# Kernel tuning notes

Hardware: AMD Instinct MI355X
Metric: run time of the kernel (lower is better)

## Reference

```python
import jax, jax.numpy as jnp
import numpy as np

B, N, F = 8, 512, 128
H, U = 4, 32
LEAKY_ALPHA = 0.2

def setup_inputs() -> dict:
    key = jax.random.key(0)
    k1, k2, k3, k4 = jax.random.split(key, 4)
    inputs = jax.random.normal(k1, (B, N, F), dtype=jnp.float32)
    # glorot-ish scaled params
    W_src = jax.random.normal(k2, (H, F, U), dtype=jnp.float32) * (2.0 / (F + U)) ** 0.5
    W_dst = jax.random.normal(k3, (H, F, U), dtype=jnp.float32) * (2.0 / (F + U)) ** 0.5
    a = jax.random.normal(k4, (H, U, 1), dtype=jnp.float32) * (2.0 / (U + 1)) ** 0.5
    return {"inputs": inputs, "W_src": W_src, "W_dst": W_dst, "a": a}

def reference(inputs, W_src, W_dst, a):
    # GATv2, eval mode (no dropout). Loop over the small fixed head count to
    # keep peak memory at one (B,N,N,U) pairwise tensor at a time, matching
    # the original per-head loop.
    outs = []
    for h in range(W_src.shape[0]):
        h_src = inputs @ W_src[h]          # (B, N, U)
        h_dst = inputs @ W_dst[h]          # (B, N, U)
        # pairwise[b,i,j,:] = h_src[b,i] + h_dst[b,j]
        pair = jax.nn.leaky_relu(h_src[:, :, None, :] + h_dst[:, None, :, :],
                                 negative_slope=LEAKY_ALPHA)  # (B,N,N,U)
        scores = jnp.einsum('biju,u->bij', pair, a[h, :, 0])   # (B,N,N)
        attn = jax.nn.softmax(scores, axis=-1)
        outs.append(attn @ h_src)          # (B,N,U) -- weighted sum of h_src
    return jnp.concatenate(outs, axis=-1)  # concat_heads=True -> (B,N,H*U)
```

## Files before the change

kernel.cpp:

```cpp
#include <hip/hip_runtime.h>
#include <hip/hip_bf16.h>

#define B_ 8
#define N_ 512
#define F_ 128
#define H_ 4
#define U_ 32
#define LEAKY_ALPHA 0.2f
#define PS 520

typedef __attribute__((ext_vector_type(8))) short short8;
typedef __attribute__((ext_vector_type(4))) short short4v;
typedef __attribute__((ext_vector_type(4))) float f32x4;

static __device__ __forceinline__ short f2bf_s(float x) {
    __hip_bfloat16 hv = __float2bfloat16(x);
    return *reinterpret_cast<short*>(&hv);
}
static __device__ __forceinline__ float bf2f_s(short v) {
    return __uint_as_float(((unsigned)(unsigned short)v) << 16);
}

__global__ __launch_bounds__(512) void proj_kernel(
    const float* __restrict__ x, const float* __restrict__ Wsrc,
    const float* __restrict__ Wdst, const float* __restrict__ a,
    float* __restrict__ hsrc, float* __restrict__ hdstNT,
    float* __restrict__ Drow, float* __restrict__ ascaled,
    short* __restrict__ hsrcT)
{
    __shared__ float4 xlds[16 * 32];
    const int t  = threadIdx.x;
    const int r0 = blockIdx.x * 16;

    xlds[t] = ((const float4*)x)[(size_t)r0 * 32 + t];
    __syncthreads();

    const int u  = t & 31;
    const int h  = (t >> 5) & 3;
    const int rq = t >> 7;
    const float* Ws = Wsrc + h * (F_ * U_) + u;
    const float* Wd = Wdst + h * (F_ * U_) + u;

    float as[4], ad[4];
#pragma unroll
    for (int r = 0; r < 4; ++r) { as[r] = 0.f; ad[r] = 0.f; }

#pragma unroll 2
    for (int fc = 0; fc < 32; ++fc) {
        const float s0 = Ws[(4 * fc + 0) * U_];
        const float s1 = Ws[(4 * fc + 1) * U_];
        const float s2 = Ws[(4 * fc + 2) * U_];
        const float s3 = Ws[(4 * fc + 3) * U_];
        const float d0 = Wd[(4 * fc + 0) * U_];
        const float d1 = Wd[(4 * fc + 1) * U_];
        const float d2 = Wd[(4 * fc + 2) * U_];
        const float d3 = Wd[(4 * fc + 3) * U_];
#pragma unroll
        for (int r = 0; r < 4; ++r) {
            const float4 xv = xlds[(rq * 4 + r) * 32 + fc];
            float vs = as[r], vd = ad[r];
            vs = fmaf(xv.x, s0, vs);  vd = fmaf(xv.x, d0, vd);
            vs = fmaf(xv.y, s1, vs);  vd = fmaf(xv.y, d1, vd);
            vs = fmaf(xv.z, s2, vs);  vd = fmaf(xv.z, d2, vd);
            vs = fmaf(xv.w, s3, vs);  vd = fmaf(xv.w, d3, vd);
            as[r] = vs; ad[r] = vd;
        }
    }

    const float av = a[h * U_ + u];
    if (t < 128 && blockIdx.x == 0)
        ascaled[h * U_ + u] = (1.f - LEAKY_ALPHA) * av;

    const int b  = r0 >> 9;
    const int n0 = (r0 & (N_ - 1)) + rq * 4;
    const int bh = b * H_ + h;

    short4v pk;
#pragma unroll
    for (int r = 0; r < 4; ++r) {
        hsrc[((size_t)(bh * N_ + n0 + r) << 5) + u] = as[r];
        pk[r] = f2bf_s(as[r]);
    }
    *(short4v*)&hsrcT[((size_t)(bh * U_) + u) * N_ + n0] = pk;

    float4 nv;
    nv.x = -ad[0]; nv.y = -ad[1]; nv.z = -ad[2]; nv.w = -ad[3];
    *(float4*)&hdstNT[((size_t)(bh * U_) + u) * N_ + n0] = nv;

#pragma unroll
    for (int r = 0; r < 4; ++r) {
        float v = ad[r] * av;
        v += __shfl_xor(v, 1);
        v += __shfl_xor(v, 2);
        v += __shfl_xor(v, 4);
        v += __shfl_xor(v, 8);
        v += __shfl_xor(v, 16);
        if (u == 0) Drow[bh * N_ + n0 + r] = v;
    }
}

__global__ __launch_bounds__(512, 4) void attn_kernel(
    const float* __restrict__ hsrc, const float* __restrict__ hdstNT,
    const float* __restrict__ Drow, const float* __restrict__ ascaled,
    const short* __restrict__ hsrcT, float* __restrict__ out)
{
    __shared__ __align__(16) short pbf[16 * PS];
    __shared__ f32x4 scr[8][64];
    __shared__ float lfin[16];

    const int t    = threadIdx.x;
    const int L    = t & 63;
    const int w    = __builtin_amdgcn_readfirstlane(t >> 6);
    const int tile = blockIdx.x & 31;
    const int bh   = blockIdx.x >> 5;
    const int h    = bh & 3;
    const int b    = bh >> 2;
    const size_t bhN = (size_t)bh * N_;
    const int ig0  = tile * 16;
    const int j    = t;

    const float* sB = hsrc + ((bhN + ig0) << 5);

    {
        const float warm = sB[t];
        asm volatile("" :: "v"(warm));
    }

    const float* dT = hdstNT + ((size_t)bh * U_) * N_ + j;
#define DL(k) float d##k = dT[(k) * N_];
    DL(0) DL(1) DL(2) DL(3) DL(4) DL(5) DL(6) DL(7)
    DL(8) DL(9) DL(10) DL(11) DL(12) DL(13) DL(14) DL(15)
    DL(16) DL(17) DL(18) DL(19) DL(20) DL(21) DL(22) DL(23)
    DL(24) DL(25) DL(26) DL(27) DL(28) DL(29) DL(30) DL(31)
#undef DL
#define PIN4(a0,a1,a2,a3) asm volatile("" : "+v"(a0), "+v"(a1), "+v"(a2), "+v"(a3));
    PIN4(d0,d1,d2,d3)     PIN4(d4,d5,d6,d7)
    PIN4(d8,d9,d10,d11)   PIN4(d12,d13,d14,d15)
    PIN4(d16,d17,d18,d19) PIN4(d20,d21,d22,d23)
    PIN4(d24,d25,d26,d27) PIN4(d28,d29,d30,d31)
#undef PIN4

    const float Dj = Drow[bhN + j];
    const float* aS = ascaled + h * U_;

#define TERM(k, dk, accv) accv = fmaf(aS[k], fmaxf(sR[k], dk), accv);
#pragma unroll 2
    for (int i = 0; i < 16; ++i) {
        const float* sR = sB + (i << 5);
        float acA = 0.f, acB = 0.f;
        TERM(0,  d0,  acA) TERM(1,  d1,  acB) TERM(2,  d2,  acA) TERM(3,  d3,  acB)
        TERM(4,  d4,  acA) TERM(5,  d5,  acB) TERM(6,  d6,  acA) TERM(7,  d7,  acB)
        TERM(8,  d8,  acA) TERM(9,  d9,  acB) TERM(10, d10, acA) TERM(11, d11, acB)
        TERM(12, d12, acA) TERM(13, d13, acB) TERM(14, d14, acA) TERM(15, d15, acB)
        TERM(16, d16, acA) TERM(17, d17, acB) TERM(18, d18, acA) TERM(19, d19, acB)
        TERM(20, d20, acA) TERM(21, d21, acB) TERM(22, d22, acA) TERM(23, d23, acB)
        TERM(24, d24, acA) TERM(25, d25, acB) TERM(26, d26, acA) TERM(27, d27, acB)
        TERM(28, d28, acA) TERM(29, d29, acB) TERM(30, d30, acA) TERM(31, d31, acB)
        const float e = __expf(Dj + acA + acB);
        pbf[i * PS + j] = f2bf_s(e);
    }
#undef TERM
    __syncthreads();

    {
        const int ri = t >> 5;
        const int rg = t & 31;
        const short8* pr = (const short8*)(pbf + ri * PS + rg * 16);
        const short8 pa = pr[0];
        const short8 pb = pr[1];
        float sum = 0.f;
#pragma unroll
        for (int k = 0; k < 8; ++k) sum += bf2f_s(pa[k]) + bf2f_s(pb[k]);
        sum += __shfl_xor(sum, 1);
        sum += __shfl_xor(sum, 2);
        sum += __shfl_xor(sum, 4);
        sum += __shfl_xor(sum, 8);
        sum += __shfl_xor(sum, 16);
        if (rg == 0) lfin[ri] = __builtin_amdgcn_rcpf(sum);
    }

    const int m  = L & 15;
    const int kq = L >> 4;
    const int nt = w & 1;
    const int ks = w >> 1;
    const short* Ap = pbf + m * PS + ks * 128 + kq * 8;
    const short* Bp = hsrcT + ((size_t)bh * U_ + nt * 16 + m) * N_ + ks * 128 + kq * 8;

    f32x4 acc = {0.f, 0.f, 0.f, 0.f};
#pragma unroll
    for (int st = 0; st < 4; ++st) {
        const short8 af = *(const short8*)(Ap + st * 32);
        const short8 bf = *(const short8*)(Bp + st * 32);
        acc = __builtin_amdgcn_mfma_f32_16x16x32_bf16(af, bf, acc, 0, 0, 0);
    }
    scr[w][L] = acc;
    __syncthreads();

    if (w < 2) {
        f32x4 s0 = scr[w][L];
        const f32x4 s1 = scr[w + 2][L];
        const f32x4 s2 = scr[w + 4][L];
        const f32x4 s3 = scr[w + 6][L];
        s0 += s1; s0 += s2; s0 += s3;
#pragma unroll
        for (int r = 0; r < 4; ++r) {
            const int il = kq * 4 + r;
            out[((size_t)(b * N_ + ig0 + il)) * (H_ * U_) + h * U_ + w * 16 + m]
                = s0[r] * lfin[il];
        }
    }
}

extern "C" void kernel_launch(void* const* d_in, const int* in_sizes, int n_in,
                              void* d_out, int out_size, void* d_ws, size_t ws_size,
                              hipStream_t stream) {
    const float* x    = (const float*)d_in[0];
    const float* Wsrc = (const float*)d_in[1];
    const float* Wdst = (const float*)d_in[2];
    const float* a    = (const float*)d_in[3];

    float* ws      = (float*)d_ws;
    float* hsrc    = ws;
    float* hdstNT  = hsrc + (size_t)B_ * H_ * N_ * U_;
    float* Drow    = hdstNT + (size_t)B_ * H_ * U_ * N_;
    float* ascaled = Drow + (size_t)B_ * H_ * N_;
    short* hsrcT   = (short*)(ascaled + H_ * U_);

    proj_kernel<<<(B_ * N_) / 16, 512, 0, stream>>>(x, Wsrc, Wdst, a,
                                                    hsrc, hdstNT, Drow, ascaled,
                                                    hsrcT);
    attn_kernel<<<B_ * H_ * (N_ / 16), 512, 0, stream>>>(hsrc, hdstNT, Drow,
                                                         ascaled, hsrcT,
                                                         (float*)d_out);
}
```

Baseline: 99.05 us.

## Split attention kernel into score pass and MFMA aggregation pass via global buffer

Splits the fused attention kernel in two. The first kernel computes the exponentiated scores and writes them as bf16 to a global workspace buffer instead of LDS. The second kernel (256 threads) reads them back to form the row sums and run the MFMA product with hsrcT. The attention coefficients a are also preloaded into registers and Dj is folded into the accumulator init. This removes LDS use and the block-level barrier from the score phase, at the cost of an extra launch and a global round trip of about 8 MB of probabilities.

```diff
diff --git a/kernel.cpp b/kernel.cpp
--- a/kernel.cpp
+++ b/kernel.cpp
@@ -7,7 +7,6 @@
 #define H_ 4
 #define U_ 32
 #define LEAKY_ALPHA 0.2f
-#define PS 520
 
 typedef __attribute__((ext_vector_type(8))) short short8;
 typedef __attribute__((ext_vector_type(4))) short short4v;
@@ -20,6 +19,7 @@
 static __device__ __forceinline__ float bf2f_s(short v) {
     return __uint_as_float(((unsigned)(unsigned short)v) << 16);
 }
+#define PINF4(v) asm volatile("" : "+v"(v.x), "+v"(v.y), "+v"(v.z), "+v"(v.w))
 
 __global__ __launch_bounds__(512) void proj_kernel(
     const float* __restrict__ x, const float* __restrict__ Wsrc,
@@ -99,32 +99,19 @@
     }
 }
 
-__global__ __launch_bounds__(512, 4) void attn_kernel(
+__global__ __launch_bounds__(512, 4) void attnA_kernel(
     const float* __restrict__ hsrc, const float* __restrict__ hdstNT,
     const float* __restrict__ Drow, const float* __restrict__ ascaled,
-    const short* __restrict__ hsrcT, float* __restrict__ out)
+    short* __restrict__ pG)
 {
-    __shared__ __align__(16) short pbf[16 * PS];
-    __shared__ f32x4 scr[8][64];
-    __shared__ float lfin[16];
-
     const int t    = threadIdx.x;
-    const int L    = t & 63;
-    const int w    = __builtin_amdgcn_readfirstlane(t >> 6);
-    const int tile = blockIdx.x & 31;
-    const int bh   = blockIdx.x >> 5;
+    const int bid  = blockIdx.x;
+    const int tile = bid & 31;
+    const int bh   = bid >> 5;
     const int h    = bh & 3;
-    const int b    = bh >> 2;
     const size_t bhN = (size_t)bh * N_;
     const int ig0  = tile * 16;
     const int j    = t;
-
-    const float* sB = hsrc + ((bhN + ig0) << 5);
-
-    {
-        const float warm = sB[t];
-        asm volatile("" :: "v"(warm));
-    }
 
     const float* dT = hdstNT + ((size_t)bh * U_) * N_ + j;
 #define DL(k) float d##k = dT[(k) * N_];
@@ -140,55 +127,92 @@
     PIN4(d24,d25,d26,d27) PIN4(d28,d29,d30,d31)
 #undef PIN4
 
+    float4 av4[8];
+    {
+        const float4* ag = (const float4*)(ascaled + h * U_);
+#pragma unroll
+        for (int q = 0; q < 8; ++q) av4[q] = ag[q];
+#pragma unroll
+        for (int q = 0; q < 8; ++q) PINF4(av4[q]);
+    }
+
     const float Dj = Drow[bhN + j];
-    const float* aS = ascaled + h * U_;
-
-#define TERM(k, dk, accv) accv = fmaf(aS[k], fmaxf(sR[k], dk), accv);
+    const float* sB = hsrc + ((bhN + ig0) << 5);
+    short* pOut = pG + (size_t)bid * (16 * N_) + j;
+
+#define T_(av, sk, dk, accv) accv = fmaf(av, fmaxf(sR[sk], dk), accv);
 #pragma unroll 2
     for (int i = 0; i < 16; ++i) {
         const float* sR = sB + (i << 5);
-        float acA = 0.f, acB = 0.f;
-        TERM(0,  d0,  acA) TERM(1,  d1,  acB) TERM(2,  d2,  acA) TERM(3,  d3,  acB)
-        TERM(4,  d4,  acA) TERM(5,  d5,  acB) TERM(6,  d6,  acA) TERM(7,  d7,  acB)
-        TERM(8,  d8,  acA) TERM(9,  d9,  acB) TERM(10, d10, acA) TERM(11, d11, acB)
-        TERM(12, d12, acA) TERM(13, d13, acB) TERM(14, d14, acA) TERM(15, d15, acB)
-        TERM(16, d16, acA) TERM(17, d17, acB) TERM(18, d18, acA) TERM(19, d19, acB)
-        TERM(20, d20, acA) TERM(21, d21, acB) TERM(22, d22, acA) TERM(23, d23, acB)
-        TERM(24, d24, acA) TERM(25, d25, acB) TERM(26, d26, acA) TERM(27, d27, acB)
-        TERM(28, d28, acA) TERM(29, d29, acB) TERM(30, d30, acA) TERM(31, d31, acB)
-        const float e = __expf(Dj + acA + acB);
-        pbf[i * PS + j] = f2bf_s(e);
-    }
-#undef TERM
-    __syncthreads();
+        float acA = Dj, acB = 0.f;
+        T_(av4[0].x, 0,  d0,  acA) T_(av4[0].y, 1,  d1,  acB)
+        T_(av4[0].z, 2,  d2,  acA) T_(av4[0].w, 3,  d3,  acB)
+        T_(av4[1].x, 4,  d4,  acA) T_(av4[1].y, 5,  d5,  acB)
+        T_(av4[1].z, 6,  d6,  acA) T_(av4[1].w, 7,  d7,  acB)
+        T_(av4[2].x, 8,  d8,  acA) T_(av4[2].y, 9,  d9,  acB)
+        T_(av4[2].z, 10, d10, acA) T_(av4[2].w, 11, d11, acB)
+        T_(av4[3].x, 12, d12, acA) T_(av4[3].y, 13, d13, acB)
+        T_(av4[3].z, 14, d14, acA) T_(av4[3].w, 15, d15, acB)
+        T_(av4[4].x, 16, d16, acA) T_(av4[4].y, 17, d17, acB)
+        T_(av4[4].z, 18, d18, acA) T_(av4[4].w, 19, d19, acB)
+        T_(av4[5].x, 20, d20, acA) T_(av4[5].y, 21, d21, acB)
+        T_(av4[5].z, 22, d22, acA) T_(av4[5].w, 23, d23, acB)
+        T_(av4[6].x, 24, d24, acA) T_(av4[6].y, 25, d25, acB)
+        T_(av4[6].z, 26, d26, acA) T_(av4[6].w, 27, d27, acB)
+        T_(av4[7].x, 28, d28, acA) T_(av4[7].y, 29, d29, acB)
+        T_(av4[7].z, 30, d30, acA) T_(av4[7].w, 31, d31, acB)
+        pOut[i * N_] = f2bf_s(__expf(acA + acB));
+    }
+#undef T_
+}
+
+__global__ __launch_bounds__(256, 4) void attnC_kernel(
+    const short* __restrict__ pG, const short* __restrict__ hsrcT,
+    float* __restrict__ out)
+{
+    __shared__ f32x4 scr[4][64];
+    __shared__ float lfin[16];
+
+    const int t    = threadIdx.x;
+    const int L    = t & 63;
+    const int w    = __builtin_amdgcn_readfirstlane(t >> 6);
+    const int bid  = blockIdx.x;
+    const int tile = bid & 31;
+    const int bh   = bid >> 5;
+    const int h    = bh & 3;
+    const int b    = bh >> 2;
+    const int ig0  = tile * 16;
+    const short* pBase = pG + (size_t)bid * (16 * N_);
 
     {
-        const int ri = t >> 5;
-        const int rg = t & 31;
-        const short8* pr = (const short8*)(pbf + ri * PS + rg * 16);
-        const short8 pa = pr[0];
-        const short8 pb = pr[1];
+        const int ri = t >> 4;
+        const int rg = t & 15;
+        const short8* pr = (const short8*)(pBase + ri * N_ + rg * 32);
         float sum = 0.f;
 #pragma unroll
-        for (int k = 0; k < 8; ++k) sum += bf2f_s(pa[k]) + bf2f_s(pb[k]);
+        for (int q = 0; q < 4; ++q) {
+            const short8 pv = pr[q];
+#pragma unroll
+            for (int k = 0; k < 8; ++k) sum += bf2f_s(pv[k]);
+        }
         sum += __shfl_xor(sum, 1);
         sum += __shfl_xor(sum, 2);
         sum += __shfl_xor(sum, 4);
         sum += __shfl_xor(sum, 8);
-        sum += __shfl_xor(sum, 16);
         if (rg == 0) lfin[ri] = __builtin_amdgcn_rcpf(sum);
     }
+    __syncthreads();
 
     const int m  = L & 15;
     const int kq = L >> 4;
     const int nt = w & 1;
     const int ks = w >> 1;
-    const short* Ap = pbf + m * PS + ks * 128 + kq * 8;
-    const short* Bp = hsrcT + ((size_t)bh * U_ + nt * 16 + m) * N_ + ks * 128 + kq * 8;
+    const short* Ap = pBase + m * N_ + ks * 256 + kq * 8;
+    const short* Bp = hsrcT + ((size_t)bh * U_ + nt * 16 + m) * N_ + ks * 256 + kq * 8;
 
     f32x4 acc = {0.f, 0.f, 0.f, 0.f};
 #pragma unroll
-    for (int st = 0; st < 4; ++st) {
+    for (int st = 0; st < 8; ++st) {
         const short8 af = *(const short8*)(Ap + st * 32);
         const short8 bf = *(const short8*)(Bp + st * 32);
         acc = __builtin_amdgcn_mfma_f32_16x16x32_bf16(af, bf, acc, 0, 0, 0);
@@ -199,9 +223,7 @@
     if (w < 2) {
         f32x4 s0 = scr[w][L];
         const f32x4 s1 = scr[w + 2][L];
-        const f32x4 s2 = scr[w + 4][L];
-        const f32x4 s3 = scr[w + 6][L];
-        s0 += s1; s0 += s2; s0 += s3;
+        s0 += s1;
 #pragma unroll
         for (int r = 0; r < 4; ++r) {
             const int il = kq * 4 + r;
@@ -225,11 +247,13 @@
     float* Drow    = hdstNT + (size_t)B_ * H_ * U_ * N_;
     float* ascaled = Drow + (size_t)B_ * H_ * N_;
     short* hsrcT   = (short*)(ascaled + H_ * U_);
+    short* pG      = hsrcT + (size_t)B_ * H_ * U_ * N_;
 
     proj_kernel<<<(B_ * N_) / 16, 512, 0, stream>>>(x, Wsrc, Wdst, a,
                                                     hsrc, hdstNT, Drow, ascaled,
                                                     hsrcT);
-    attn_kernel<<<B_ * H_ * (N_ / 16), 512, 0, stream>>>(hsrc, hdstNT, Drow,
-                                                         ascaled, hsrcT,
-                                                         (float*)d_out);
-}
+    attnA_kernel<<<B_ * H_ * (N_ / 16), 512, 0, stream>>>(hsrc, hdstNT, Drow,
+                                                          ascaled, pG);
+    attnC_kernel<<<B_ * H_ * (N_ / 16), 256, 0, stream>>>(pG, hsrcT,
+                                                          (float*)d_out);
+}
```

Result: slower. 113.4 us (+14.5%).
